# Performance work log

Hardware: AMD Instinct MI355X
Metric: run time of the kernel (lower is better)

## Reference

```python
import jax, jax.numpy as jnp
import numpy as np

SIZE = 7
SIGMA = 1.5
CHANNELS = 1
K1 = 0.01
K2 = 0.03
NP_ = SIZE * SIZE
COV_NORM = NP_ / (NP_ - 1)


def gaussian_window(size=SIZE, sigma=SIGMA, channels=CHANNELS):
    x = jnp.arange(size, dtype=jnp.float32) - size // 2
    g = jnp.exp(-x ** 2 / (2.0 * sigma ** 2))[None, :]  # [1, size]
    w = (g.T @ g)  # [size, size]
    w = w / jnp.sum(w)
    return jnp.broadcast_to(w[None, None], (channels, 1, size, size))  # [C,1,k,k]


def _blur(x, w, pad):
    # depthwise conv2d, groups == channels
    return jax.lax.conv_general_dilated(
        x, w, window_strides=(1, 1), padding=[(pad, pad), (pad, pad)],
        dimension_numbers=('NCHW', 'OIHW', 'NCHW'),
        feature_group_count=x.shape[1])


def setup_inputs() -> dict:
    key = jax.random.key(0)
    k1, k2 = jax.random.split(key)
    B, C, H, W = 64, CHANNELS, 512, 512
    X = jax.random.uniform(k1, (B, C, H, W), dtype=jnp.float32)
    Y = jax.random.uniform(k2, (B, C, H, W), dtype=jnp.float32)
    window = gaussian_window()
    return {"X": X, "Y": Y, "window": window}


def reference(X, Y, window):
    B = Y.shape[0]
    Yf = Y.reshape(B, -1)
    data_range = (jnp.max(Yf, axis=1) - jnp.min(Yf, axis=1)).reshape(B, 1, 1, 1)
    C1 = (K1 * data_range) ** 2
    C2 = (K2 * data_range) ** 2
    pad = SIZE // 2
    mux = _blur(X, window, pad)
    muy = _blur(Y, window, pad)
    mux_sq = mux * mux
    muy_sq = muy * muy
    muxy = mux * muy
    sigmax_sq = (_blur(X * X, window, pad) - mux_sq) * COV_NORM
    sigmay_sq = (_blur(Y * Y, window, pad) - muy_sq) * COV_NORM
    sigmaxy = (_blur(X * Y, window, pad) - muxy) * COV_NORM
    ssim_map = (2 * muxy + C1) * (2 * sigmaxy + C2) / ((mux_sq + muy_sq + C1) * (sigmax_sq + sigmay_sq + C2))
    return 1.0 - jnp.mean(ssim_map)
```

## Files before the change

### kernel.cpp

```cpp
#include <hip/hip_runtime.h>
#include <math.h>


__device__ __forceinline__ unsigned fkey(float f) {
    unsigned u = __float_as_uint(f);
    return (u & 0x80000000u) ? ~u : (u | 0x80000000u);
}
__device__ __forceinline__ float funkey(unsigned k) {
    return __uint_as_float((k & 0x80000000u) ? (k & 0x7FFFFFFFu) : ~k);
}

__global__ void init_ws(const float* __restrict__ w, float* __restrict__ u7,
                        unsigned* __restrict__ mink, unsigned* __restrict__ maxk,
                        double* __restrict__ sum) {
    int t = threadIdx.x;
    if (t == 0) *sum = 0.0;
    if (t < 64) { mink[t] = 0xFFFFFFFFu; maxk[t] = 0u; }
    if (t < 7) {
        float s = 0.f;
        for (int j = 0; j < 7; ++j) s += w[t * 7 + j];
        u7[t] = s;
    }
}

__global__ __launch_bounds__(256) void minmax_kernel(const float4* __restrict__ Y,
                                                     unsigned* __restrict__ mink,
                                                     unsigned* __restrict__ maxk) {
    int b = blockIdx.x >> 3, ch = blockIdx.x & 7;
    const float4* p = Y + (size_t)b * 65536 + (size_t)ch * 8192 + threadIdx.x;
    float lmin = INFINITY, lmax = -INFINITY;
#pragma unroll
    for (int i = 0; i < 32; ++i) {
        float4 v = p[(size_t)i * 256];
        lmin = fminf(lmin, fminf(fminf(v.x, v.y), fminf(v.z, v.w)));
        lmax = fmaxf(lmax, fmaxf(fmaxf(v.x, v.y), fmaxf(v.z, v.w)));
    }
#pragma unroll
    for (int off = 32; off; off >>= 1) {
        lmin = fminf(lmin, __shfl_down(lmin, off));
        lmax = fmaxf(lmax, __shfl_down(lmax, off));
    }
    if ((threadIdx.x & 63) == 0) {
        atomicMin(&mink[b], fkey(lmin));
        atomicMax(&maxk[b], fkey(lmax));
    }
}

__global__ __launch_bounds__(256) void ssim_kernel(const float* __restrict__ X,
                                                   const float* __restrict__ Yg,
                                                   const float* __restrict__ u7,
                                                   const unsigned* __restrict__ mink,
                                                   const unsigned* __restrict__ maxk,
                                                   double* __restrict__ sum) {
    __shared__ float xs[2][264];
    __shared__ float ys[2][264];
    __shared__ float warpsum[4];

    const int blk = blockIdx.x;
    const int b = blk >> 4;
    const int sub = blk & 15;
    const int cs = sub & 1;
    const int rs = sub >> 1;
    const int c0 = cs * 256;
    const int r0 = rs * 64;
    const int t = threadIdx.x;

    float u[7];
#pragma unroll
    for (int i = 0; i < 7; ++i) u[i] = u7[i];

    const float dr = funkey(maxk[b]) - funkey(mink[b]);
    float C1 = 0.01f * dr; C1 *= C1;
    float C2 = 0.03f * dr; C2 *= C2;
    const float cn = 49.f / 48.f;

    const float* __restrict__ Xb = X  + (size_t)b * 262144;
    const float* __restrict__ Yb = Yg + (size_t)b * 262144;

    float px[7], py[7], pxx[7], pyy[7], pxy[7];
#pragma unroll
    for (int k = 0; k < 7; ++k) { px[k]=0.f; py[k]=0.f; pxx[k]=0.f; pyy[k]=0.f; pxy[k]=0.f; }

    float ssacc = 0.f;

    auto load_row = [&](int r, int p) {
        {
            int l = t;
            int c = c0 - 3 + l;
            float xv = 0.f, yv = 0.f;
            if (r >= 0 && r < 512 && c >= 0 && c < 512) {
                xv = Xb[r * 512 + c];
                yv = Yb[r * 512 + c];
            }
            xs[p][l] = xv; ys[p][l] = yv;
        }
        if (t < 6) {
            int l = 256 + t;
            int c = c0 - 3 + l;
            float xv = 0.f, yv = 0.f;
            if (r >= 0 && r < 512 && c < 512) {
                xv = Xb[r * 512 + c];
                yv = Yb[r * 512 + c];
            }
            xs[p][l] = xv; ys[p][l] = yv;
        }
    };

    load_row(r0 - 3, 0);
    __syncthreads();

    for (int j = 0; j < 70; ++j) {
        const int p = j & 1;
        if (j < 69) load_row(r0 - 3 + j + 1, p ^ 1);

        float hx = 0.f, hy = 0.f, hxx = 0.f, hyy = 0.f, hxy = 0.f;
#pragma unroll
        for (int k = 0; k < 7; ++k) {
            float xv = xs[p][t + k];
            float yv = ys[p][t + k];
            float wx = u[k] * xv;
            float wy = u[k] * yv;
            hx += wx;
            hy += wy;
            hxx = fmaf(wx, xv, hxx);
            hxy = fmaf(wx, yv, hxy);
            hyy = fmaf(wy, yv, hyy);
        }

#pragma unroll
        for (int k = 0; k < 6; ++k) {
            px[k] = px[k + 1]; py[k] = py[k + 1];
            pxx[k] = pxx[k + 1]; pyy[k] = pyy[k + 1]; pxy[k] = pxy[k + 1];
        }
        px[6] = hx; py[6] = hy; pxx[6] = hxx; pyy[6] = hyy; pxy[6] = hxy;

        if (j >= 6) {
            float mux = 0.f, muy = 0.f, mxx = 0.f, myy = 0.f, mxy = 0.f;
#pragma unroll
            for (int k = 0; k < 7; ++k) {
                mux = fmaf(u[k], px[k], mux);
                muy = fmaf(u[k], py[k], muy);
                mxx = fmaf(u[k], pxx[k], mxx);
                myy = fmaf(u[k], pyy[k], myy);
                mxy = fmaf(u[k], pxy[k], mxy);
            }
            float mux2 = mux * mux, muy2 = muy * muy, muxy = mux * muy;
            float sxx = (mxx - mux2) * cn;
            float syy = (myy - muy2) * cn;
            float sxy = (mxy - muxy) * cn;
            float num = (2.f * muxy + C1) * (2.f * sxy + C2);
            float den = (mux2 + muy2 + C1) * (sxx + syy + C2);
            ssacc += num / den;
        }
        __syncthreads();
    }

#pragma unroll
    for (int off = 32; off; off >>= 1) ssacc += __shfl_down(ssacc, off);
    if ((t & 63) == 0) warpsum[t >> 6] = ssacc;
    __syncthreads();
    if (t == 0) {
        double s = (double)warpsum[0] + (double)warpsum[1] +
                   (double)warpsum[2] + (double)warpsum[3];
        atomicAdd(sum, s);
    }
}

__global__ void finalize_kernel(const double* __restrict__ sum, float* __restrict__ out) {
    out[0] = (float)(1.0 - (*sum) / (64.0 * 512.0 * 512.0));
}

extern "C" void kernel_launch(void* const* d_in, const int* in_sizes, int n_in,
                              void* d_out, int out_size, void* d_ws, size_t ws_size,
                              hipStream_t stream) {
    const float* X = (const float*)d_in[0];
    const float* Y = (const float*)d_in[1];
    const float* W = (const float*)d_in[2];

    char* ws = (char*)d_ws;
    double* sum = (double*)(ws + 0);
    unsigned* mink = (unsigned*)(ws + 16);
    unsigned* maxk = (unsigned*)(ws + 16 + 256);
    float* u7 = (float*)(ws + 16 + 512);

    init_ws<<<1, 64, 0, stream>>>(W, u7, mink, maxk, sum);
    minmax_kernel<<<512, 256, 0, stream>>>((const float4*)Y, mink, maxk);
    ssim_kernel<<<1024, 256, 0, stream>>>(X, Y, u7, mink, maxk, sum);
    finalize_kernel<<<1, 1, 0, stream>>>(sum, (float*)d_out);
}
```

Before: 111.6 us.

## Batch seven row loads per barrier with ring-buffered SSIM row pipeline

Restructures the SSIM kernel so each block loads seven rows into a shared float2 ring buffer, then computes seven output rows per barrier pair instead of syncing once per row. Horizontal blur results go in a register ring indexed modulo 7, which avoids the per-row shift of the old history arrays. The change also halves the row tile to 32, doubling the grid for both kernels, clamps load addresses instead of branching, and replaces the division with a fast reciprocal. The costs are more redundant halo rows per block, since 6 halo rows are reloaded for every 32 output rows, and a small loss of accuracy from the approximate reciprocal.

```diff
diff --git a/kernel.cpp b/kernel.cpp
--- a/kernel.cpp
+++ b/kernel.cpp
@@ -26,11 +26,11 @@
 __global__ __launch_bounds__(256) void minmax_kernel(const float4* __restrict__ Y,
                                                      unsigned* __restrict__ mink,
                                                      unsigned* __restrict__ maxk) {
-    int b = blockIdx.x >> 3, ch = blockIdx.x & 7;
-    const float4* p = Y + (size_t)b * 65536 + (size_t)ch * 8192 + threadIdx.x;
+    int b = blockIdx.x >> 4, ch = blockIdx.x & 15;
+    const float4* p = Y + (size_t)b * 65536 + (size_t)ch * 4096 + threadIdx.x;
     float lmin = INFINITY, lmax = -INFINITY;
 #pragma unroll
-    for (int i = 0; i < 32; ++i) {
+    for (int i = 0; i < 16; ++i) {
         float4 v = p[(size_t)i * 256];
         lmin = fminf(lmin, fminf(fminf(v.x, v.y), fminf(v.z, v.w)));
         lmax = fmaxf(lmax, fmaxf(fmaxf(v.x, v.y), fmaxf(v.z, v.w)));
@@ -46,24 +46,23 @@
     }
 }
 
-__global__ __launch_bounds__(256) void ssim_kernel(const float* __restrict__ X,
-                                                   const float* __restrict__ Yg,
-                                                   const float* __restrict__ u7,
-                                                   const unsigned* __restrict__ mink,
-                                                   const unsigned* __restrict__ maxk,
-                                                   double* __restrict__ sum) {
-    __shared__ float xs[2][264];
-    __shared__ float ys[2][264];
+__global__ __launch_bounds__(256, 6) void ssim_kernel(const float* __restrict__ X,
+                                                      const float* __restrict__ Yg,
+                                                      const float* __restrict__ u7,
+                                                      const unsigned* __restrict__ mink,
+                                                      const unsigned* __restrict__ maxk,
+                                                      double* __restrict__ sum) {
+    __shared__ float2 s[7][264];
     __shared__ float warpsum[4];
 
     const int blk = blockIdx.x;
-    const int b = blk >> 4;
-    const int sub = blk & 15;
-    const int cs = sub & 1;
-    const int rs = sub >> 1;
-    const int c0 = cs * 256;
-    const int r0 = rs * 64;
-    const int t = threadIdx.x;
+    const int b   = blk >> 5;
+    const int sub = blk & 31;
+    const int cs  = sub & 1;
+    const int rs  = sub >> 1;
+    const int c0  = cs * 256;
+    const int r0  = rs * 32;
+    const int t   = threadIdx.x;
 
     float u[7];
 #pragma unroll
@@ -77,92 +76,101 @@
     const float* __restrict__ Xb = X  + (size_t)b * 262144;
     const float* __restrict__ Yb = Yg + (size_t)b * 262144;
 
-    float px[7], py[7], pxx[7], pyy[7], pxy[7];
-#pragma unroll
-    for (int k = 0; k < 7; ++k) { px[k]=0.f; py[k]=0.f; pxx[k]=0.f; pyy[k]=0.f; pxy[k]=0.f; }
+    const int  c1   = c0 - 3 + t;
+    const int  cc1  = min(max(c1, 0), 511);
+    const bool cok1 = (c1 >= 0) && (c1 < 512);
+    const bool tail = (t < 6);
+    const int  c2   = c0 + 253 + t;
+    const int  cc2  = min(c2, 511);
+    const bool cok2 = (c2 < 512);
+
+    float phx[7], phy[7], phxx[7], phyy[7], phxy[7];
 
     float ssacc = 0.f;
 
-    auto load_row = [&](int r, int p) {
-        {
-            int l = t;
-            int c = c0 - 3 + l;
-            float xv = 0.f, yv = 0.f;
-            if (r >= 0 && r < 512 && c >= 0 && c < 512) {
-                xv = Xb[r * 512 + c];
-                yv = Yb[r * 512 + c];
-            }
-            xs[p][l] = xv; ys[p][l] = yv;
-        }
-        if (t < 6) {
-            int l = 256 + t;
-            int c = c0 - 3 + l;
-            float xv = 0.f, yv = 0.f;
-            if (r >= 0 && r < 512 && c < 512) {
-                xv = Xb[r * 512 + c];
-                yv = Yb[r * 512 + c];
-            }
-            xs[p][l] = xv; ys[p][l] = yv;
+    auto load_row = [&](int j, int slot) {
+        int  r   = r0 - 3 + j;
+        bool rok = (r >= 0) && (r < 512);
+        int  rr  = min(max(r, 0), 511);
+        const float* xp = Xb + (size_t)rr * 512;
+        const float* yp = Yb + (size_t)rr * 512;
+        float xv = xp[cc1], yv = yp[cc1];
+        bool ok = rok && cok1;
+        s[slot][t] = make_float2(ok ? xv : 0.f, ok ? yv : 0.f);
+        if (tail) {
+            float xv2 = xp[cc2], yv2 = yp[cc2];
+            bool ok2 = rok && cok2;
+            s[slot][256 + t] = make_float2(ok2 ? xv2 : 0.f, ok2 ? yv2 : 0.f);
         }
     };
 
-    load_row(r0 - 3, 0);
-    __syncthreads();
-
-    for (int j = 0; j < 70; ++j) {
-        const int p = j & 1;
-        if (j < 69) load_row(r0 - 3 + j + 1, p ^ 1);
-
+    auto hblur = [&](int bufslot, int pslot) {
         float hx = 0.f, hy = 0.f, hxx = 0.f, hyy = 0.f, hxy = 0.f;
 #pragma unroll
         for (int k = 0; k < 7; ++k) {
-            float xv = xs[p][t + k];
-            float yv = ys[p][t + k];
-            float wx = u[k] * xv;
-            float wy = u[k] * yv;
-            hx += wx;
-            hy += wy;
-            hxx = fmaf(wx, xv, hxx);
-            hxy = fmaf(wx, yv, hxy);
-            hyy = fmaf(wy, yv, hyy);
+            float2 v = s[bufslot][t + k];
+            float wx = u[k] * v.x;
+            float wy = u[k] * v.y;
+            hx += wx; hy += wy;
+            hxx = fmaf(wx, v.x, hxx);
+            hxy = fmaf(wx, v.y, hxy);
+            hyy = fmaf(wy, v.y, hyy);
         }
+        phx[pslot] = hx; phy[pslot] = hy;
+        phxx[pslot] = hxx; phyy[pslot] = hyy; phxy[pslot] = hxy;
+    };
+
+    auto emit = [&](int jj) {
+        hblur(jj, (6 + jj) % 7);
+        float mux = 0.f, muy = 0.f, mxx = 0.f, myy = 0.f, mxy = 0.f;
+#pragma unroll
+        for (int k = 0; k < 7; ++k) {
+            const int sl = (jj + k) % 7;
+            mux = fmaf(u[k], phx[sl], mux);
+            muy = fmaf(u[k], phy[sl], muy);
+            mxx = fmaf(u[k], phxx[sl], mxx);
+            myy = fmaf(u[k], phyy[sl], myy);
+            mxy = fmaf(u[k], phxy[sl], mxy);
+        }
+        float mux2 = mux * mux, muy2 = muy * muy, muxy = mux * muy;
+        float sxx = (mxx - mux2) * cn;
+        float syy = (myy - muy2) * cn;
+        float sxy = (mxy - muxy) * cn;
+        float num = (2.f * muxy + C1) * (2.f * sxy + C2);
+        float den = (mux2 + muy2 + C1) * (sxx + syy + C2);
+        ssacc = fmaf(num, __builtin_amdgcn_rcpf(den), ssacc);
+    };
 
 #pragma unroll
-        for (int k = 0; k < 6; ++k) {
-            px[k] = px[k + 1]; py[k] = py[k + 1];
-            pxx[k] = pxx[k + 1]; pyy[k] = pyy[k + 1]; pxy[k] = pxy[k + 1];
-        }
-        px[6] = hx; py[6] = hy; pxx[6] = hxx; pyy[6] = hyy; pxy[6] = hxy;
+    for (int j = 0; j < 6; ++j) load_row(j, j);
+    __syncthreads();
+#pragma unroll
+    for (int j = 0; j < 6; ++j) hblur(j, j);
+    __syncthreads();
 
-        if (j >= 6) {
-            float mux = 0.f, muy = 0.f, mxx = 0.f, myy = 0.f, mxy = 0.f;
+    for (int g = 0; g < 4; ++g) {
+        const int jbase = 6 + 7 * g;
 #pragma unroll
-            for (int k = 0; k < 7; ++k) {
-                mux = fmaf(u[k], px[k], mux);
-                muy = fmaf(u[k], py[k], muy);
-                mxx = fmaf(u[k], pxx[k], mxx);
-                myy = fmaf(u[k], pyy[k], myy);
-                mxy = fmaf(u[k], pxy[k], mxy);
-            }
-            float mux2 = mux * mux, muy2 = muy * muy, muxy = mux * muy;
-            float sxx = (mxx - mux2) * cn;
-            float syy = (myy - muy2) * cn;
-            float sxy = (mxy - muxy) * cn;
-            float num = (2.f * muxy + C1) * (2.f * sxy + C2);
-            float den = (mux2 + muy2 + C1) * (sxx + syy + C2);
-            ssacc += num / den;
-        }
+        for (int jj = 0; jj < 7; ++jj) load_row(jbase + jj, jj);
+        __syncthreads();
+#pragma unroll
+        for (int jj = 0; jj < 7; ++jj) emit(jj);
         __syncthreads();
     }
+#pragma unroll
+    for (int jj = 0; jj < 4; ++jj) load_row(34 + jj, jj);
+    __syncthreads();
+#pragma unroll
+    for (int jj = 0; jj < 4; ++jj) emit(jj);
 
 #pragma unroll
     for (int off = 32; off; off >>= 1) ssacc += __shfl_down(ssacc, off);
     if ((t & 63) == 0) warpsum[t >> 6] = ssacc;
     __syncthreads();
     if (t == 0) {
-        double s = (double)warpsum[0] + (double)warpsum[1] +
-                   (double)warpsum[2] + (double)warpsum[3];
-        atomicAdd(sum, s);
+        double sm = (double)warpsum[0] + (double)warpsum[1] +
+                    (double)warpsum[2] + (double)warpsum[3];
+        atomicAdd(sum, sm);
     }
 }
 
@@ -184,7 +192,7 @@
     float* u7 = (float*)(ws + 16 + 512);
 
     init_ws<<<1, 64, 0, stream>>>(W, u7, mink, maxk, sum);
-    minmax_kernel<<<512, 256, 0, stream>>>((const float4*)Y, mink, maxk);
-    ssim_kernel<<<1024, 256, 0, stream>>>(X, Y, u7, mink, maxk, sum);
+    minmax_kernel<<<1024, 256, 0, stream>>>((const float4*)Y, mink, maxk);
+    ssim_kernel<<<2048, 256, 0, stream>>>(X, Y, u7, mink, maxk, sum);
     finalize_kernel<<<1, 1, 0, stream>>>(sum, (float*)d_out);
 }
```

Result: slower. 241.0 us (+115.9%).
